# Optimization experiments

Hardware: AMD Instinct MI355X
Metric: run time of the kernel (lower is better)

Reference implementation:

```python
import jax, jax.numpy as jnp
import numpy as np

TOP_K = 2
B, S, H, I, E = 1, 2048, 1024, 4096, 8


def setup_inputs() -> dict:
    key = jax.random.key(0)
    k1, k2, k3, k4 = jax.random.split(key, 4)
    x = jax.random.normal(k1, (B, S, H), dtype=jnp.float32)
    gate_w = jax.random.normal(k2, (E, H), dtype=jnp.float32)
    w1 = jax.random.normal(k3, (E, I, H), dtype=jnp.float32)
    w2 = jax.random.normal(k4, (E, H, I), dtype=jnp.float32)
    return {"x": x, "gate_w": gate_w, "w1": w1, "w2": w2}


def reference(x, gate_w, w1, w2):
    b, s, h = x.shape
    xf = x.reshape(-1, h)                      # [T, H]
    T = xf.shape[0]
    logits = xf @ gate_w.T                     # [T, E]
    probs = jax.nn.softmax(logits, axis=-1)
    wts, idx = jax.lax.top_k(probs, TOP_K)     # [T, k]
    wts = wts / jnp.sum(wts, axis=-1, keepdims=True)
    # combine[t, e] = routing weight of expert e for token t (0 if not selected)
    combine = jnp.zeros((T, w1.shape[0]), dtype=x.dtype)
    combine = combine.at[jnp.arange(T)[:, None], idx].add(wts)
    # dense dispatch: every expert processes every token, masked/weighted by combine
    hid = jax.nn.silu(jnp.einsum('th,eih->tei', xf, w1))   # [T, E, I]
    y = jnp.einsum('tei,ehi->teh', hid, w2)                # [T, E, H]
    out = jnp.einsum('teh,te->th', y, combine)             # [T, H]
    return out.reshape(b, s, h)
```

## Files before the change

kernel.cpp:

```cpp
#include <hip/hip_runtime.h>
#include <stdint.h>

#define TT 2048
#define HH 1024
#define II 4096
#define EE 8

typedef __attribute__((ext_vector_type(4))) float floatx4;
typedef __attribute__((ext_vector_type(8))) __bf16 bf16x8;

__device__ __forceinline__ unsigned short f2bf(float f) {
  union { float f; unsigned u; } v; v.f = f;
  return (unsigned short)((v.u + 0x7FFFu + ((v.u >> 16) & 1u)) >> 16);
}

__device__ __forceinline__ void async_ld16(const void* g, void* l) {
  __builtin_amdgcn_global_load_lds(
      (__attribute__((address_space(1))) void*)g,
      (__attribute__((address_space(3))) void*)l, 16, 0, 0);
}

__global__ __launch_bounds__(256) void k_gating(
    const float* __restrict__ x, const float* __restrict__ gw,
    unsigned short* __restrict__ xb, int* __restrict__ sel_e,
    float* __restrict__ sel_w, int* __restrict__ counts) {
  int t = blockIdx.x;
  int tid = threadIdx.x;
  floatx4 xv = ((const floatx4*)(x + (size_t)t * HH))[tid];
  ushort4 xo;
  xo.x = f2bf(xv.x); xo.y = f2bf(xv.y); xo.z = f2bf(xv.z); xo.w = f2bf(xv.w);
  ((ushort4*)(xb + (size_t)t * HH))[tid] = xo;

  float part[EE];
#pragma unroll
  for (int e = 0; e < EE; e++) {
    floatx4 g = ((const floatx4*)(gw + e * HH))[tid];
    part[e] = xv.x * g.x + xv.y * g.y + xv.z * g.z + xv.w * g.w;
  }
#pragma unroll
  for (int e = 0; e < EE; e++) {
    float v = part[e];
#pragma unroll
    for (int off = 32; off > 0; off >>= 1) v += __shfl_down(v, off, 64);
    part[e] = v;
  }
  __shared__ float red[4][EE];
  int wave = tid >> 6;
  if ((tid & 63) == 0) {
#pragma unroll
    for (int e = 0; e < EE; e++) red[wave][e] = part[e];
  }
  __syncthreads();
  if (tid == 0) {
    float lg[EE];
#pragma unroll
    for (int e = 0; e < EE; e++)
      lg[e] = red[0][e] + red[1][e] + red[2][e] + red[3][e];
    int e0 = 0;
#pragma unroll
    for (int e = 1; e < EE; e++) if (lg[e] > lg[e0]) e0 = e;
    int e1 = (e0 == 0) ? 1 : 0;
#pragma unroll
    for (int e = 0; e < EE; e++) if (e != e0 && lg[e] > lg[e1]) e1 = e;
    float w0 = 1.f / (1.f + expf(lg[e1] - lg[e0]));
    sel_e[t * 2] = e0; sel_e[t * 2 + 1] = e1;
    sel_w[t * 2] = w0; sel_w[t * 2 + 1] = 1.f - w0;
    atomicAdd(&counts[e0], 1);
    atomicAdd(&counts[e1], 1);
  }
}

__global__ __launch_bounds__(256) void k_fill(
    const int* __restrict__ counts, const int* __restrict__ sel_e,
    const float* __restrict__ sel_w, int* __restrict__ bases,
    int* __restrict__ row_token, float* __restrict__ row_w,
    int* __restrict__ inv_slot) {
  __shared__ int lb[EE];
  __shared__ int lc[EE];
  int tid = threadIdx.x;
  if (tid == 0) {
    int s = 0;
    for (int e = 0; e < EE; e++) { lb[e] = s; s += counts[e]; }
  }
  if (tid < EE) lc[tid] = 0;
  __syncthreads();
  for (int p = tid; p < TT * 2; p += 256) {
    int e = sel_e[p];
    int slot = lb[e] + atomicAdd(&lc[e], 1);
    row_token[slot] = p >> 1;
    row_w[slot] = sel_w[p];
    inv_slot[p] = slot;
  }
  __syncthreads();
  if (tid < EE) bases[tid] = lb[tid];
}

__global__ __launch_bounds__(256) void k_convert(
    const float* __restrict__ w1, const float* __restrict__ w2,
    unsigned short* __restrict__ w1b, unsigned short* __restrict__ w2b) {
  const int half_blocks = (int)(((size_t)EE * II * HH) / (256 * 8));
  const float* s;
  unsigned short* d;
  int b = blockIdx.x;
  if (b < half_blocks) { s = w1; d = w1b; } else { s = w2; d = w2b; b -= half_blocks; }
  size_t i = ((size_t)b * 256 + threadIdx.x) * 8;
  floatx4 v0 = *(const floatx4*)(s + i);
  floatx4 v1 = *(const floatx4*)(s + i + 4);
  uint4 o;
  o.x = (unsigned)f2bf(v0.x) | ((unsigned)f2bf(v0.y) << 16);
  o.y = (unsigned)f2bf(v0.z) | ((unsigned)f2bf(v0.w) << 16);
  o.z = (unsigned)f2bf(v1.x) | ((unsigned)f2bf(v1.y) << 16);
  o.w = (unsigned)f2bf(v1.z) | ((unsigned)f2bf(v1.w) << 16);
  *(uint4*)(d + i) = o;
}

__global__ __launch_bounds__(256, 3) void k_gemm1(
    const unsigned short* __restrict__ xb,
    const unsigned short* __restrict__ w1b,
    unsigned short* __restrict__ hid,
    const int* __restrict__ counts, const int* __restrict__ bases,
    const int* __restrict__ row_token) {
  const int e = blockIdx.z;
  const int count = counts[e];
  const int m0 = blockIdx.y * 128;
  if (m0 >= count) return;
  const int n0 = blockIdx.x * 128;
  const int base = bases[e];

  __shared__ __align__(16) unsigned short Smem[128 * 32 * 2];
  unsigned short* As = Smem;
  unsigned short* Bs = Smem + 128 * 32;

  const int tid = threadIdx.x;
  const int lane = tid & 63;
  const int wave = tid >> 6;
  const int wm = (wave & 1) * 64;
  const int wn = (wave >> 1) * 64;
  const int quad = lane >> 4;
  const int l16 = lane & 15;

  const int rA0 = tid >> 2;
  const int rA1 = rA0 + 64;
  const int cc = (tid & 3) * 8;

  int g0 = m0 + rA0; if (g0 > count - 1) g0 = count - 1;
  int g1 = m0 + rA1; if (g1 > count - 1) g1 = count - 1;
  const unsigned short* aS0 = xb + (size_t)row_token[base + g0] * HH + cc;
  const unsigned short* aS1 = xb + (size_t)row_token[base + g1] * HH + cc;
  const unsigned short* wp = w1b + (size_t)e * II * HH;
  const unsigned short* bS0 = wp + (size_t)(n0 + rA0) * HH + cc;
  const unsigned short* bS1 = wp + (size_t)(n0 + rA1) * HH + cc;

  unsigned short* lA0 = As + tid * 8;
  unsigned short* lA1 = As + tid * 8 + 2048;
  unsigned short* lB0 = Bs + tid * 8;
  unsigned short* lB1 = Bs + tid * 8 + 2048;

  const floatx4 fz = {0.f, 0.f, 0.f, 0.f};
  floatx4 acc[4][4];
#pragma unroll
  for (int i = 0; i < 4; i++)
#pragma unroll
    for (int j = 0; j < 4; j++) acc[i][j] = fz;

  for (int k0 = 0; k0 < HH; k0 += 32) {
    async_ld16(aS0 + k0, lA0);
    async_ld16(aS1 + k0, lA1);
    async_ld16(bS0 + k0, lB0);
    async_ld16(bS1 + k0, lB1);
    __syncthreads();
    bf16x8 af[4], bfr[4];
#pragma unroll
    for (int i = 0; i < 4; i++) {
      af[i]  = *(const bf16x8*)(As + (wm + i * 16 + l16) * 32 + quad * 8);
      bfr[i] = *(const bf16x8*)(Bs + (wn + i * 16 + l16) * 32 + quad * 8);
    }
#pragma unroll
    for (int i = 0; i < 4; i++)
#pragma unroll
      for (int j = 0; j < 4; j++)
        acc[i][j] = __builtin_amdgcn_mfma_f32_16x16x32_bf16(af[i], bfr[j], acc[i][j], 0, 0, 0);
    __syncthreads();
  }

  unsigned short* Sl = Smem + wave * (16 * 72);
#pragma unroll
  for (int i = 0; i < 4; i++) {
#pragma unroll
    for (int r = 0; r < 4; r++) {
      const int row16 = quad * 4 + r;
#pragma unroll
      for (int j = 0; j < 4; j++) {
        float z = acc[i][j][r];
        Sl[row16 * 72 + l16 + 16 * j] = f2bf(z / (1.f + __expf(-z)));
      }
    }
#pragma unroll
    for (int half = 0; half < 2; half++) {
      const int row16 = (lane >> 3) + 8 * half;
      const int m = wm + i * 16 + row16;
      if (m0 + m < count) {
        bf16x8 v = *(const bf16x8*)(Sl + row16 * 72 + (lane & 7) * 8);
        *(bf16x8*)(hid + (size_t)(base + m0 + m) * II + n0 + wn + (lane & 7) * 8) = v;
      }
    }
  }
}

__global__ __launch_bounds__(256, 3) void k_gemm2(
    const unsigned short* __restrict__ hid,
    const unsigned short* __restrict__ w2b,
    float* __restrict__ yp,
    const int* __restrict__ counts, const int* __restrict__ bases) {
  const int e = blockIdx.z;
  const int count = counts[e];
  const int m0 = blockIdx.y * 128;
  if (m0 >= count) return;
  const int nt = blockIdx.x & 7;
  const int ks = blockIdx.x >> 3;
  const int n0 = nt * 128;
  const int base = bases[e];

  __shared__ __align__(16) unsigned short Smem2[128 * 32 * 2];
  unsigned short* As = Smem2;
  unsigned short* Bs = Smem2 + 128 * 32;

  const int tid = threadIdx.x;
  const int lane = tid & 63;
  const int wave = tid >> 6;
  const int wm = (wave & 1) * 64;
  const int wn = (wave >> 1) * 64;
  const int quad = lane >> 4;
  const int l16 = lane & 15;

  const int rA0 = tid >> 2;
  const int rA1 = rA0 + 64;
  const int cc = (tid & 3) * 8;

  int g0 = m0 + rA0; if (g0 > count - 1) g0 = count - 1;
  int g1 = m0 + rA1; if (g1 > count - 1) g1 = count - 1;
  const unsigned short* aS0 = hid + (size_t)(base + g0) * II + cc;
  const unsigned short* aS1 = hid + (size_t)(base + g1) * II + cc;
  const unsigned short* wp = w2b + (size_t)e * HH * II;
  const unsigned short* bS0 = wp + (size_t)(n0 + rA0) * II + cc;
  const unsigned short* bS1 = wp + (size_t)(n0 + rA1) * II + cc;

  unsigned short* lA0 = As + tid * 8;
  unsigned short* lA1 = As + tid * 8 + 2048;
  unsigned short* lB0 = Bs + tid * 8;
  unsigned short* lB1 = Bs + tid * 8 + 2048;

  const floatx4 fz = {0.f, 0.f, 0.f, 0.f};
  floatx4 acc[4][4];
#pragma unroll
  for (int i = 0; i < 4; i++)
#pragma unroll
    for (int j = 0; j < 4; j++) acc[i][j] = fz;

  const int kbeg = ks * (II / 2);
  const int kend = kbeg + II / 2;
  for (int k0 = kbeg; k0 < kend; k0 += 32) {
    async_ld16(aS0 + k0, lA0);
    async_ld16(aS1 + k0, lA1);
    async_ld16(bS0 + k0, lB0);
    async_ld16(bS1 + k0, lB1);
    __syncthreads();
    bf16x8 af[4], bfr[4];
#pragma unroll
    for (int i = 0; i < 4; i++) {
      af[i]  = *(const bf16x8*)(As + (wm + i * 16 + l16) * 32 + quad * 8);
      bfr[i] = *(const bf16x8*)(Bs + (wn + i * 16 + l16) * 32 + quad * 8);
    }
#pragma unroll
    for (int i = 0; i < 4; i++)
#pragma unroll
      for (int j = 0; j < 4; j++)
        acc[i][j] = __builtin_amdgcn_mfma_f32_16x16x32_bf16(af[i], bfr[j], acc[i][j], 0, 0, 0);
    __syncthreads();
  }

#pragma unroll
  for (int i = 0; i < 4; i++) {
#pragma unroll
    for (int r = 0; r < 4; r++) {
      const int m = wm + i * 16 + quad * 4 + r;
      if (m0 + m < count) {
        float* op = yp + ((size_t)ks * (TT * 2) + base + m0 + m) * HH + n0 + wn + l16;
#pragma unroll
        for (int j = 0; j < 4; j++) op[j * 16] = acc[i][j][r];
      }
    }
  }
}

__global__ __launch_bounds__(256) void k_combine(
    const float* __restrict__ yp, const int* __restrict__ inv_slot,
    const float* __restrict__ sel_w, float* __restrict__ out) {
  const int t = blockIdx.x;
  const int tid = threadIdx.x;
  const int s0 = inv_slot[2 * t];
  const int s1 = inv_slot[2 * t + 1];
  const float w0 = sel_w[2 * t];
  const float w1 = sel_w[2 * t + 1];
  const floatx4 a0 = ((const floatx4*)(yp + (size_t)s0 * HH))[tid];
  const floatx4 a1 = ((const floatx4*)(yp + ((size_t)(TT * 2) + s0) * HH))[tid];
  const floatx4 b0 = ((const floatx4*)(yp + (size_t)s1 * HH))[tid];
  const floatx4 b1 = ((const floatx4*)(yp + ((size_t)(TT * 2) + s1) * HH))[tid];
  floatx4 v = w0 * (a0 + a1) + w1 * (b0 + b1);
  ((floatx4*)(out + (size_t)t * HH))[tid] = v;
}

extern "C" void kernel_launch(void* const* d_in, const int* in_sizes, int n_in,
                              void* d_out, int out_size, void* d_ws, size_t ws_size,
                              hipStream_t stream) {
  const float* x  = (const float*)d_in[0];
  const float* gw = (const float*)d_in[1];
  const float* w1 = (const float*)d_in[2];
  const float* w2 = (const float*)d_in[3];
  float* out = (float*)d_out;

  char* ws = (char*)d_ws;
  size_t off = 0;
  auto take = [&](size_t n) -> char* {
    char* p = ws + off;
    off += (n + 255) & ~(size_t)255;
    return p;
  };
  unsigned short* xb  = (unsigned short*)take((size_t)TT * HH * 2);
  unsigned short* w1b = (unsigned short*)take((size_t)EE * II * HH * 2);
  unsigned short* w2b = (unsigned short*)take((size_t)EE * HH * II * 2);
  unsigned short* hid = (unsigned short*)take((size_t)TT * 2 * II * 2);
  int*   counts    = (int*)take(EE * 4);
  int*   bases     = (int*)take(EE * 4);
  int*   row_token = (int*)take((size_t)TT * 2 * 4);
  float* row_w     = (float*)take((size_t)TT * 2 * 4);
  int*   sel_e     = (int*)take((size_t)TT * 2 * 4);
  float* sel_w     = (float*)take((size_t)TT * 2 * 4);
  int*   inv_slot  = (int*)take((size_t)TT * 2 * 4);
  if (off > ws_size) return;

  float* yp = (float*)w1b;

  hipMemsetAsync(counts, 0, EE * 4, stream);

  k_gating<<<TT, 256, 0, stream>>>(x, gw, xb, sel_e, sel_w, counts);
  k_fill<<<1, 256, 0, stream>>>(counts, sel_e, sel_w, bases, row_token, row_w, inv_slot);
  {
    const int half_blocks = (int)(((size_t)EE * II * HH) / (256 * 8));
    k_convert<<<2 * half_blocks, 256, 0, stream>>>(w1, w2, w1b, w2b);
  }
  k_gemm1<<<dim3(II / 128, 16, EE), 256, 0, stream>>>(xb, w1b, hid, counts, bases, row_token);
  k_gemm2<<<dim3(16, 16, EE), 256, 0, stream>>>(hid, w2b, yp, counts, bases);
  k_combine<<<TT, 256, 0, stream>>>(yp, inv_slot, sel_w, out);
}
```

Baseline: 517.1 us.

## Fuse fp32-to-bf16 weight conversion into GEMM loads and raise GEMM2 split-K to 4

Drops the separate weight conversion kernel. Both GEMMs now read the fp32 expert weights directly, convert them to bf16 in registers, and store them to LDS, prefetching the next K tile one step ahead. This removes a full read and write pass over all weights. The cost is that each M-tile block re-reads the fp32 weights, which doubles the bytes fetched per block, and register pressure rises. GEMM2 split-K goes from 2 to 4 to add parallelism, with a separate yp buffer and a combine kernel that sums four partials.

Result: faster. 468.9 us (-9.3%).

```diff
diff --git a/kernel.cpp b/kernel.cpp
--- a/kernel.cpp
+++ b/kernel.cpp
@@ -5,6 +5,7 @@
 #define HH 1024
 #define II 4096
 #define EE 8
+#define KS 4
 
 typedef __attribute__((ext_vector_type(4))) float floatx4;
 typedef __attribute__((ext_vector_type(8))) __bf16 bf16x8;
@@ -95,28 +96,9 @@
   if (tid < EE) bases[tid] = lb[tid];
 }
 
-__global__ __launch_bounds__(256) void k_convert(
-    const float* __restrict__ w1, const float* __restrict__ w2,
-    unsigned short* __restrict__ w1b, unsigned short* __restrict__ w2b) {
-  const int half_blocks = (int)(((size_t)EE * II * HH) / (256 * 8));
-  const float* s;
-  unsigned short* d;
-  int b = blockIdx.x;
-  if (b < half_blocks) { s = w1; d = w1b; } else { s = w2; d = w2b; b -= half_blocks; }
-  size_t i = ((size_t)b * 256 + threadIdx.x) * 8;
-  floatx4 v0 = *(const floatx4*)(s + i);
-  floatx4 v1 = *(const floatx4*)(s + i + 4);
-  uint4 o;
-  o.x = (unsigned)f2bf(v0.x) | ((unsigned)f2bf(v0.y) << 16);
-  o.y = (unsigned)f2bf(v0.z) | ((unsigned)f2bf(v0.w) << 16);
-  o.z = (unsigned)f2bf(v1.x) | ((unsigned)f2bf(v1.y) << 16);
-  o.w = (unsigned)f2bf(v1.z) | ((unsigned)f2bf(v1.w) << 16);
-  *(uint4*)(d + i) = o;
-}
-
-__global__ __launch_bounds__(256, 3) void k_gemm1(
+__global__ __launch_bounds__(256) void k_gemm1(
     const unsigned short* __restrict__ xb,
-    const unsigned short* __restrict__ w1b,
+    const float* __restrict__ w1,
     unsigned short* __restrict__ hid,
     const int* __restrict__ counts, const int* __restrict__ bases,
     const int* __restrict__ row_token) {
@@ -147,9 +129,9 @@
   int g1 = m0 + rA1; if (g1 > count - 1) g1 = count - 1;
   const unsigned short* aS0 = xb + (size_t)row_token[base + g0] * HH + cc;
   const unsigned short* aS1 = xb + (size_t)row_token[base + g1] * HH + cc;
-  const unsigned short* wp = w1b + (size_t)e * II * HH;
-  const unsigned short* bS0 = wp + (size_t)(n0 + rA0) * HH + cc;
-  const unsigned short* bS1 = wp + (size_t)(n0 + rA1) * HH + cc;
+  const float* wp = w1 + (size_t)e * II * HH;
+  const float* bp0 = wp + (size_t)(n0 + rA0) * HH + cc;
+  const float* bp1 = wp + (size_t)(n0 + rA1) * HH + cc;
 
   unsigned short* lA0 = As + tid * 8;
   unsigned short* lA1 = As + tid * 8 + 2048;
@@ -163,12 +145,29 @@
 #pragma unroll
     for (int j = 0; j < 4; j++) acc[i][j] = fz;
 
+  floatx4 f0a = *(const floatx4*)(bp0);
+  floatx4 f0b = *(const floatx4*)(bp0 + 4);
+  floatx4 f1a = *(const floatx4*)(bp1);
+  floatx4 f1b = *(const floatx4*)(bp1 + 4);
+
   for (int k0 = 0; k0 < HH; k0 += 32) {
+    bf16x8 wv0, wv1;
+#pragma unroll
+    for (int j = 0; j < 4; j++) {
+      wv0[j] = (__bf16)f0a[j]; wv0[j + 4] = (__bf16)f0b[j];
+      wv1[j] = (__bf16)f1a[j]; wv1[j + 4] = (__bf16)f1b[j];
+    }
+    *(bf16x8*)lB0 = wv0;
+    *(bf16x8*)lB1 = wv1;
     async_ld16(aS0 + k0, lA0);
     async_ld16(aS1 + k0, lA1);
-    async_ld16(bS0 + k0, lB0);
-    async_ld16(bS1 + k0, lB1);
     __syncthreads();
+    if (k0 + 32 < HH) {
+      f0a = *(const floatx4*)(bp0 + k0 + 32);
+      f0b = *(const floatx4*)(bp0 + k0 + 36);
+      f1a = *(const floatx4*)(bp1 + k0 + 32);
+      f1b = *(const floatx4*)(bp1 + k0 + 36);
+    }
     bf16x8 af[4], bfr[4];
 #pragma unroll
     for (int i = 0; i < 4; i++) {
@@ -207,9 +206,9 @@
   }
 }
 
-__global__ __launch_bounds__(256, 3) void k_gemm2(
+__global__ __launch_bounds__(256) void k_gemm2(
     const unsigned short* __restrict__ hid,
-    const unsigned short* __restrict__ w2b,
+    const float* __restrict__ w2,
     float* __restrict__ yp,
     const int* __restrict__ counts, const int* __restrict__ bases) {
   const int e = blockIdx.z;
@@ -241,9 +240,9 @@
   int g1 = m0 + rA1; if (g1 > count - 1) g1 = count - 1;
   const unsigned short* aS0 = hid + (size_t)(base + g0) * II + cc;
   const unsigned short* aS1 = hid + (size_t)(base + g1) * II + cc;
-  const unsigned short* wp = w2b + (size_t)e * HH * II;
-  const unsigned short* bS0 = wp + (size_t)(n0 + rA0) * II + cc;
-  const unsigned short* bS1 = wp + (size_t)(n0 + rA1) * II + cc;
+  const float* wp = w2 + (size_t)e * HH * II;
+  const float* bp0 = wp + (size_t)(n0 + rA0) * II + cc;
+  const float* bp1 = wp + (size_t)(n0 + rA1) * II + cc;
 
   unsigned short* lA0 = As + tid * 8;
   unsigned short* lA1 = As + tid * 8 + 2048;
@@ -257,14 +256,32 @@
 #pragma unroll
     for (int j = 0; j < 4; j++) acc[i][j] = fz;
 
-  const int kbeg = ks * (II / 2);
-  const int kend = kbeg + II / 2;
+  const int kbeg = ks * (II / KS);
+  const int kend = kbeg + II / KS;
+
+  floatx4 f0a = *(const floatx4*)(bp0 + kbeg);
+  floatx4 f0b = *(const floatx4*)(bp0 + kbeg + 4);
+  floatx4 f1a = *(const floatx4*)(bp1 + kbeg);
+  floatx4 f1b = *(const floatx4*)(bp1 + kbeg + 4);
+
   for (int k0 = kbeg; k0 < kend; k0 += 32) {
+    bf16x8 wv0, wv1;
+#pragma unroll
+    for (int j = 0; j < 4; j++) {
+      wv0[j] = (__bf16)f0a[j]; wv0[j + 4] = (__bf16)f0b[j];
+      wv1[j] = (__bf16)f1a[j]; wv1[j + 4] = (__bf16)f1b[j];
+    }
+    *(bf16x8*)lB0 = wv0;
+    *(bf16x8*)lB1 = wv1;
     async_ld16(aS0 + k0, lA0);
     async_ld16(aS1 + k0, lA1);
-    async_ld16(bS0 + k0, lB0);
-    async_ld16(bS1 + k0, lB1);
     __syncthreads();
+    if (k0 + 32 < kend) {
+      f0a = *(const floatx4*)(bp0 + k0 + 32);
+      f0b = *(const floatx4*)(bp0 + k0 + 36);
+      f1a = *(const floatx4*)(bp1 + k0 + 32);
+      f1b = *(const floatx4*)(bp1 + k0 + 36);
+    }
     bf16x8 af[4], bfr[4];
 #pragma unroll
     for (int i = 0; i < 4; i++) {
@@ -302,11 +319,14 @@
   const int s1 = inv_slot[2 * t + 1];
   const float w0 = sel_w[2 * t];
   const float w1 = sel_w[2 * t + 1];
-  const floatx4 a0 = ((const floatx4*)(yp + (size_t)s0 * HH))[tid];
-  const floatx4 a1 = ((const floatx4*)(yp + ((size_t)(TT * 2) + s0) * HH))[tid];
-  const floatx4 b0 = ((const floatx4*)(yp + (size_t)s1 * HH))[tid];
-  const floatx4 b1 = ((const floatx4*)(yp + ((size_t)(TT * 2) + s1) * HH))[tid];
-  floatx4 v = w0 * (a0 + a1) + w1 * (b0 + b1);
+  floatx4 a = {0.f, 0.f, 0.f, 0.f};
+  floatx4 b = {0.f, 0.f, 0.f, 0.f};
+#pragma unroll
+  for (int ks = 0; ks < KS; ks++) {
+    a += ((const floatx4*)(yp + ((size_t)ks * (TT * 2) + s0) * HH))[tid];
+    b += ((const floatx4*)(yp + ((size_t)ks * (TT * 2) + s1) * HH))[tid];
+  }
+  floatx4 v = w0 * a + w1 * b;
   ((floatx4*)(out + (size_t)t * HH))[tid] = v;
 }
 
@@ -327,9 +347,8 @@
     return p;
   };
   unsigned short* xb  = (unsigned short*)take((size_t)TT * HH * 2);
-  unsigned short* w1b = (unsigned short*)take((size_t)EE * II * HH * 2);
-  unsigned short* w2b = (unsigned short*)take((size_t)EE * HH * II * 2);
   unsigned short* hid = (unsigned short*)take((size_t)TT * 2 * II * 2);
+  float* yp = (float*)take((size_t)KS * (TT * 2) * HH * 4);
   int*   counts    = (int*)take(EE * 4);
   int*   bases     = (int*)take(EE * 4);
   int*   row_token = (int*)take((size_t)TT * 2 * 4);
@@ -339,17 +358,11 @@
   int*   inv_slot  = (int*)take((size_t)TT * 2 * 4);
   if (off > ws_size) return;
 
-  float* yp = (float*)w1b;
-
   hipMemsetAsync(counts, 0, EE * 4, stream);
 
   k_gating<<<TT, 256, 0, stream>>>(x, gw, xb, sel_e, sel_w, counts);
   k_fill<<<1, 256, 0, stream>>>(counts, sel_e, sel_w, bases, row_token, row_w, inv_slot);
-  {
-    const int half_blocks = (int)(((size_t)EE * II * HH) / (256 * 8));
-    k_convert<<<2 * half_blocks, 256, 0, stream>>>(w1, w2, w1b, w2b);
-  }
-  k_gemm1<<<dim3(II / 128, 16, EE), 256, 0, stream>>>(xb, w1b, hid, counts, bases, row_token);
-  k_gemm2<<<dim3(16, 16, EE), 256, 0, stream>>>(hid, w2b, yp, counts, bases);
+  k_gemm1<<<dim3(II / 128, 16, EE), 256, 0, stream>>>(xb, w1, hid, counts, bases, row_token);
+  k_gemm2<<<dim3(8 * KS, 16, EE), 256, 0, stream>>>(hid, w2, yp, counts, bases);
   k_combine<<<TT, 256, 0, stream>>>(yp, inv_slot, sel_w, out);
 }
```
